# Kernel tuning notes

Measured on AMD Instinct MI355X. Metric: run time of the kernel, lower is better.

## Reference

```python
import jax, jax.numpy as jnp
import numpy as np

T = 131072  # timesteps
D = 256     # state_dim


def setup_inputs() -> dict:
    key = jax.random.key(0)
    kA, kB = jax.random.split(key)
    A = jax.random.normal(kA, (T, D), dtype=jnp.float32)
    Bu = jax.random.normal(kB, (T, D), dtype=jnp.float32)
    return {"A": A, "Bu": Bu}


def reference(A, Bu):
    # S5 associative scan combinator over (A, Bu) pairs along time axis 0:
    #   (A_i, Bu_i) * (A_j, Bu_j) = (A_j * A_i, A_j * Bu_i + Bu_j)
    def s5_operator(x, y):
        A_i, Bu_i = x
        A_j, Bu_j = y
        return (A_j * A_i, A_j * Bu_i + Bu_j)

    return jax.lax.associative_scan(s5_operator, (A, Bu), axis=0)
```

## Files before the change

### kernel.cpp

```cpp
#include <hip/hip_runtime.h>


#define T_TOTAL 131072
#define D_DIM   256
#define CHUNK   32
#define NCHUNK  (T_TOTAL / CHUNK)
#define NSUPER  64
#define SLEN    (NCHUNK / NSUPER)
#define NTHR    (D_DIM / 4)

typedef float vfloat4 __attribute__((ext_vector_type(4)));

__device__ __forceinline__ void combine(float4& ra, float4& rb,
                                        const float4 ga, const float4 gb) {
    rb.x = fmaf(ga.x, rb.x, gb.x);  ra.x = ga.x * ra.x;
    rb.y = fmaf(ga.y, rb.y, gb.y);  ra.y = ga.y * ra.y;
    rb.z = fmaf(ga.z, rb.z, gb.z);  ra.z = ga.z * ra.z;
    rb.w = fmaf(ga.w, rb.w, gb.w);  ra.w = ga.w * ra.w;
}

__device__ __forceinline__ void nt_store4(float* p, const float4 v) {
    vfloat4 t = {v.x, v.y, v.z, v.w};
    __builtin_nontemporal_store(t, (vfloat4*)p);
}

__global__ __launch_bounds__(NTHR) void s5_pass1(
    const float* __restrict__ A, const float* __restrict__ Bu,
    float* __restrict__ aggA, float* __restrict__ aggB)
{
    const int c  = blockIdx.x;
    const int ch = threadIdx.x * 4;
    const size_t base = (size_t)c * CHUNK * D_DIM + ch;

    float4 a = make_float4(1.f, 1.f, 1.f, 1.f);
    float4 b = make_float4(0.f, 0.f, 0.f, 0.f);

    #pragma unroll 8
    for (int t = 0; t < CHUNK; ++t) {
        const float4 at = *(const float4*)(A  + base + (size_t)t * D_DIM);
        const float4 bt = *(const float4*)(Bu + base + (size_t)t * D_DIM);
        combine(a, b, at, bt);
    }
    *(float4*)(aggA + (size_t)c * D_DIM + ch) = a;
    *(float4*)(aggB + (size_t)c * D_DIM + ch) = b;
}

__global__ __launch_bounds__(NTHR) void s5_pass2a(
    float* __restrict__ aggA, float* __restrict__ aggB,
    float* __restrict__ supA, float* __restrict__ supB)
{
    const int s  = blockIdx.x;
    const int ch = threadIdx.x * 4;

    float4 ra = make_float4(1.f, 1.f, 1.f, 1.f);
    float4 rb = make_float4(0.f, 0.f, 0.f, 0.f);

    for (int i = 0; i < SLEN; ++i) {
        const size_t o = (size_t)(s * SLEN + i) * D_DIM + ch;
        const float4 ga = *(const float4*)(aggA + o);
        const float4 gb = *(const float4*)(aggB + o);
        *(float4*)(aggA + o) = ra;
        *(float4*)(aggB + o) = rb;
        combine(ra, rb, ga, gb);
    }
    *(float4*)(supA + (size_t)s * D_DIM + ch) = ra;
    *(float4*)(supB + (size_t)s * D_DIM + ch) = rb;
}

__global__ __launch_bounds__(NTHR) void s5_pass2b(
    float* __restrict__ supA, float* __restrict__ supB)
{
    const int ch = threadIdx.x * 4;
    float4 ra = make_float4(1.f, 1.f, 1.f, 1.f);
    float4 rb = make_float4(0.f, 0.f, 0.f, 0.f);

    for (int s = 0; s < NSUPER; ++s) {
        const size_t o = (size_t)s * D_DIM + ch;
        const float4 ga = *(const float4*)(supA + o);
        const float4 gb = *(const float4*)(supB + o);
        *(float4*)(supA + o) = ra;
        *(float4*)(supB + o) = rb;
        combine(ra, rb, ga, gb);
    }
}

__global__ __launch_bounds__(NTHR) void s5_pass3(
    const float* __restrict__ A, const float* __restrict__ Bu,
    const float* __restrict__ relA, const float* __restrict__ relB,
    const float* __restrict__ supA, const float* __restrict__ supB,
    float* __restrict__ outA, float* __restrict__ outB)
{
    const int c  = blockIdx.x;
    const int ch = threadIdx.x * 4;
    const int s  = c / SLEN;

    const size_t co = (size_t)c * D_DIM + ch;
    const size_t so = (size_t)s * D_DIM + ch;

    const float4 rA = *(const float4*)(relA + co);
    const float4 rB = *(const float4*)(relB + co);
    const float4 sA = *(const float4*)(supA + so);
    const float4 sB = *(const float4*)(supB + so);

    float4 ra, rb;
    rb.x = fmaf(rA.x, sB.x, rB.x);  ra.x = rA.x * sA.x;
    rb.y = fmaf(rA.y, sB.y, rB.y);  ra.y = rA.y * sA.y;
    rb.z = fmaf(rA.z, sB.z, rB.z);  ra.z = rA.z * sA.z;
    rb.w = fmaf(rA.w, sB.w, rB.w);  ra.w = rA.w * sA.w;

    const size_t base = (size_t)c * CHUNK * D_DIM + ch;

    #pragma unroll 8
    for (int t = 0; t < CHUNK; ++t) {
        const size_t o = base + (size_t)t * D_DIM;
        const float4 at = *(const float4*)(A  + o);
        const float4 bt = *(const float4*)(Bu + o);
        combine(ra, rb, at, bt);
        nt_store4(outA + o, ra);
        nt_store4(outB + o, rb);
    }
}

extern "C" void kernel_launch(void* const* d_in, const int* in_sizes, int n_in,
                              void* d_out, int out_size, void* d_ws, size_t ws_size,
                              hipStream_t stream)
{
    const float* A  = (const float*)d_in[0];
    const float* Bu = (const float*)d_in[1];
    float* outA = (float*)d_out;
    float* outB = (float*)d_out + (size_t)T_TOTAL * D_DIM;

    float* aggA = (float*)d_ws;
    float* aggB = aggA + (size_t)NCHUNK * D_DIM;
    float* supA = aggB + (size_t)NCHUNK * D_DIM;
    float* supB = supA + (size_t)NSUPER * D_DIM;

    s5_pass1 <<<NCHUNK, NTHR, 0, stream>>>(A, Bu, aggA, aggB);
    s5_pass2a<<<NSUPER, NTHR, 0, stream>>>(aggA, aggB, supA, supB);
    s5_pass2b<<<1,      NTHR, 0, stream>>>(supA, supB);
    s5_pass3 <<<NCHUNK, NTHR, 0, stream>>>(A, Bu, aggA, aggB, supA, supB, outA, outB);
}
```

Measured before the change: 492.3 us.

## Replace three-pass scan with single-pass decoupled look-back scan

```diff
diff --git a/kernel.cpp b/kernel.cpp
--- a/kernel.cpp
+++ b/kernel.cpp
@@ -3,121 +3,172 @@
 
 #define T_TOTAL 131072
 #define D_DIM   256
-#define CHUNK   32
-#define NCHUNK  (T_TOTAL / CHUNK)
-#define NSUPER  64
-#define SLEN    (NCHUNK / NSUPER)
-#define NTHR    (D_DIM / 4)
+#define RPW     16
+#define WAVES   4
+#define RPB     (RPW * WAVES)
+#define NCHUNK  (T_TOTAL / RPB)
+#define NTHR    (WAVES * 64)
+
+#define F_NONE 0
+#define F_AGG  1
+#define F_PRE  2
 
 typedef float vfloat4 __attribute__((ext_vector_type(4)));
 
-__device__ __forceinline__ void combine(float4& ra, float4& rb,
-                                        const float4 ga, const float4 gb) {
-    rb.x = fmaf(ga.x, rb.x, gb.x);  ra.x = ga.x * ra.x;
-    rb.y = fmaf(ga.y, rb.y, gb.y);  ra.y = ga.y * ra.y;
-    rb.z = fmaf(ga.z, rb.z, gb.z);  ra.z = ga.z * ra.z;
-    rb.w = fmaf(ga.w, rb.w, gb.w);  ra.w = ga.w * ra.w;
+__device__ __forceinline__ float4 nt_load4(const float* p) {
+    vfloat4 t = __builtin_nontemporal_load((const vfloat4*)p);
+    return make_float4(t.x, t.y, t.z, t.w);
 }
-
 __device__ __forceinline__ void nt_store4(float* p, const float4 v) {
     vfloat4 t = {v.x, v.y, v.z, v.w};
     __builtin_nontemporal_store(t, (vfloat4*)p);
 }
 
-__global__ __launch_bounds__(NTHR) void s5_pass1(
-    const float* __restrict__ A, const float* __restrict__ Bu,
-    float* __restrict__ aggA, float* __restrict__ aggB)
-{
-    const int c  = blockIdx.x;
-    const int ch = threadIdx.x * 4;
-    const size_t base = (size_t)c * CHUNK * D_DIM + ch;
-
-    float4 a = make_float4(1.f, 1.f, 1.f, 1.f);
-    float4 b = make_float4(0.f, 0.f, 0.f, 0.f);
-
-    #pragma unroll 8
-    for (int t = 0; t < CHUNK; ++t) {
-        const float4 at = *(const float4*)(A  + base + (size_t)t * D_DIM);
-        const float4 bt = *(const float4*)(Bu + base + (size_t)t * D_DIM);
-        combine(a, b, at, bt);
-    }
-    *(float4*)(aggA + (size_t)c * D_DIM + ch) = a;
-    *(float4*)(aggB + (size_t)c * D_DIM + ch) = b;
+__device__ __forceinline__ void append(float4& ra, float4& rb,
+                                       const float4 ga, const float4 gb) {
+    rb.x = fmaf(ga.x, rb.x, gb.x);  ra.x *= ga.x;
+    rb.y = fmaf(ga.y, rb.y, gb.y);  ra.y *= ga.y;
+    rb.z = fmaf(ga.z, rb.z, gb.z);  ra.z *= ga.z;
+    rb.w = fmaf(ga.w, rb.w, gb.w);  ra.w *= ga.w;
+}
+__device__ __forceinline__ void prepend(float4& aa, float4& ab,
+                                        const float4 ga, const float4 gb) {
+    ab.x = fmaf(aa.x, gb.x, ab.x);  aa.x *= ga.x;
+    ab.y = fmaf(aa.y, gb.y, ab.y);  aa.y *= ga.y;
+    ab.z = fmaf(aa.z, gb.z, ab.z);  aa.z *= ga.z;
+    ab.w = fmaf(aa.w, gb.w, ab.w);  aa.w *= ga.w;
 }
 
-__global__ __launch_bounds__(NTHR) void s5_pass2a(
-    float* __restrict__ aggA, float* __restrict__ aggB,
-    float* __restrict__ supA, float* __restrict__ supB)
+__global__ __launch_bounds__(256) void s5_init(int* __restrict__ flags)
 {
-    const int s  = blockIdx.x;
-    const int ch = threadIdx.x * 4;
-
-    float4 ra = make_float4(1.f, 1.f, 1.f, 1.f);
-    float4 rb = make_float4(0.f, 0.f, 0.f, 0.f);
-
-    for (int i = 0; i < SLEN; ++i) {
-        const size_t o = (size_t)(s * SLEN + i) * D_DIM + ch;
-        const float4 ga = *(const float4*)(aggA + o);
-        const float4 gb = *(const float4*)(aggB + o);
-        *(float4*)(aggA + o) = ra;
-        *(float4*)(aggB + o) = rb;
-        combine(ra, rb, ga, gb);
-    }
-    *(float4*)(supA + (size_t)s * D_DIM + ch) = ra;
-    *(float4*)(supB + (size_t)s * D_DIM + ch) = rb;
+    const int i = blockIdx.x * 256 + threadIdx.x;
+    if (i <= NCHUNK) flags[i] = F_NONE;
 }
 
-__global__ __launch_bounds__(NTHR) void s5_pass2b(
-    float* __restrict__ supA, float* __restrict__ supB)
+__global__ __launch_bounds__(NTHR, 2) void s5_scan(
+    const float* __restrict__ A, const float* __restrict__ Bu,
+    float* __restrict__ outA, float* __restrict__ outB,
+    float* __restrict__ aggA, float* __restrict__ aggB,
+    float* __restrict__ preA, float* __restrict__ preB,
+    int* __restrict__ flags, int* __restrict__ ticket)
 {
-    const int ch = threadIdx.x * 4;
-    float4 ra = make_float4(1.f, 1.f, 1.f, 1.f);
-    float4 rb = make_float4(0.f, 0.f, 0.f, 0.f);
+    __shared__ float lsA[WAVES][D_DIM];
+    __shared__ float lsB[WAVES][D_DIM];
+    __shared__ float lpA[D_DIM];
+    __shared__ float lpB[D_DIM];
+    __shared__ int   s_chunk;
 
-    for (int s = 0; s < NSUPER; ++s) {
-        const size_t o = (size_t)s * D_DIM + ch;
-        const float4 ga = *(const float4*)(supA + o);
-        const float4 gb = *(const float4*)(supB + o);
-        *(float4*)(supA + o) = ra;
-        *(float4*)(supB + o) = rb;
-        combine(ra, rb, ga, gb);
+    const int tid  = threadIdx.x;
+    if (tid == 0) s_chunk = atomicAdd(ticket, 1);
+    __syncthreads();
+    const int chunk = s_chunk;
+    const int wave  = tid >> 6;
+    const int lane  = tid & 63;
+    const int ch    = lane * 4;
+
+    const size_t base = (size_t)(chunk * RPB + wave * RPW) * D_DIM + ch;
+
+    float4 la[RPW], lb[RPW];
+    #pragma unroll
+    for (int t = 0; t < RPW; ++t) {
+        la[t] = nt_load4(A  + base + (size_t)t * D_DIM);
+        lb[t] = nt_load4(Bu + base + (size_t)t * D_DIM);
     }
-}
 
-__global__ __launch_bounds__(NTHR) void s5_pass3(
-    const float* __restrict__ A, const float* __restrict__ Bu,
-    const float* __restrict__ relA, const float* __restrict__ relB,
-    const float* __restrict__ supA, const float* __restrict__ supB,
-    float* __restrict__ outA, float* __restrict__ outB)
-{
-    const int c  = blockIdx.x;
-    const int ch = threadIdx.x * 4;
-    const int s  = c / SLEN;
+    #pragma unroll
+    for (int t = 1; t < RPW; ++t) {
+        lb[t].x = fmaf(la[t].x, lb[t-1].x, lb[t].x);  la[t].x *= la[t-1].x;
+        lb[t].y = fmaf(la[t].y, lb[t-1].y, lb[t].y);  la[t].y *= la[t-1].y;
+        lb[t].z = fmaf(la[t].z, lb[t-1].z, lb[t].z);  la[t].z *= la[t-1].z;
+        lb[t].w = fmaf(la[t].w, lb[t-1].w, lb[t].w);  la[t].w *= la[t-1].w;
+    }
 
-    const size_t co = (size_t)c * D_DIM + ch;
-    const size_t so = (size_t)s * D_DIM + ch;
+    *(float4*)&lsA[wave][ch] = la[RPW - 1];
+    *(float4*)&lsB[wave][ch] = lb[RPW - 1];
+    __syncthreads();
 
-    const float4 rA = *(const float4*)(relA + co);
-    const float4 rB = *(const float4*)(relB + co);
-    const float4 sA = *(const float4*)(supA + so);
-    const float4 sB = *(const float4*)(supB + so);
+    float4 wpa = make_float4(1.f, 1.f, 1.f, 1.f);
+    float4 wpb = make_float4(0.f, 0.f, 0.f, 0.f);
+    #pragma unroll
+    for (int w = 0; w < WAVES - 1; ++w) {
+        if (wave > w)
+            append(wpa, wpb, *(const float4*)&lsA[w][ch],
+                             *(const float4*)&lsB[w][ch]);
+    }
 
-    float4 ra, rb;
-    rb.x = fmaf(rA.x, sB.x, rB.x);  ra.x = rA.x * sA.x;
-    rb.y = fmaf(rA.y, sB.y, rB.y);  ra.y = rA.y * sA.y;
-    rb.z = fmaf(rA.z, sB.z, rB.z);  ra.z = rA.z * sA.z;
-    rb.w = fmaf(rA.w, sB.w, rB.w);  ra.w = rA.w * sA.w;
+    if (wave == 3 && chunk > 0) {
+        float4 ba = wpa, bb = wpb;
+        append(ba, bb, la[RPW - 1], lb[RPW - 1]);
+        *(float4*)(aggA + (size_t)chunk * D_DIM + ch) = ba;
+        *(float4*)(aggB + (size_t)chunk * D_DIM + ch) = bb;
+        __threadfence();
+        if (lane == 0)
+            __hip_atomic_fetch_max(&flags[chunk], F_AGG,
+                                   __ATOMIC_RELEASE, __HIP_MEMORY_SCOPE_AGENT);
+    }
 
-    const size_t base = (size_t)c * CHUNK * D_DIM + ch;
+    if (wave == 0) {
+        float4 ba = make_float4(1.f, 1.f, 1.f, 1.f);
+        float4 bb = make_float4(0.f, 0.f, 0.f, 0.f);
+        #pragma unroll
+        for (int w = 0; w < WAVES; ++w)
+            append(ba, bb, *(const float4*)&lsA[w][ch],
+                           *(const float4*)&lsB[w][ch]);
 
-    #pragma unroll 8
-    for (int t = 0; t < CHUNK; ++t) {
-        const size_t o = base + (size_t)t * D_DIM;
-        const float4 at = *(const float4*)(A  + o);
-        const float4 bt = *(const float4*)(Bu + o);
-        combine(ra, rb, at, bt);
-        nt_store4(outA + o, ra);
-        nt_store4(outB + o, rb);
+        float4 Pa = make_float4(1.f, 1.f, 1.f, 1.f);
+        float4 Pb = make_float4(0.f, 0.f, 0.f, 0.f);
+        if (chunk > 0) {
+            int k = chunk - 1;
+            for (;;) {
+                int f;
+                for (;;) {
+                    f = __hip_atomic_load(&flags[k], __ATOMIC_ACQUIRE,
+                                          __HIP_MEMORY_SCOPE_AGENT);
+                    f = __builtin_amdgcn_readfirstlane(f);
+                    if (f != F_NONE) break;
+                    __builtin_amdgcn_s_sleep(1);
+                }
+                if (f == F_AGG) {
+                    const float4 ga = *(const float4*)(aggA + (size_t)k * D_DIM + ch);
+                    const float4 gb = *(const float4*)(aggB + (size_t)k * D_DIM + ch);
+                    prepend(Pa, Pb, ga, gb);
+                    --k;
+                } else {
+                    const float4 ga = *(const float4*)(preA + (size_t)k * D_DIM + ch);
+                    const float4 gb = *(const float4*)(preB + (size_t)k * D_DIM + ch);
+                    prepend(Pa, Pb, ga, gb);
+                    break;
+                }
+            }
+        }
+
+        float4 ia = Pa, ib = Pb;
+        append(ia, ib, ba, bb);
+        *(float4*)(preA + (size_t)chunk * D_DIM + ch) = ia;
+        *(float4*)(preB + (size_t)chunk * D_DIM + ch) = ib;
+        __threadfence();
+        if (lane == 0)
+            __hip_atomic_fetch_max(&flags[chunk], F_PRE,
+                                   __ATOMIC_RELEASE, __HIP_MEMORY_SCOPE_AGENT);
+
+        *(float4*)&lpA[ch] = Pa;
+        *(float4*)&lpB[ch] = Pb;
+    }
+    __syncthreads();
+
+    float4 fpA = *(const float4*)&lpA[ch];
+    float4 fpB = *(const float4*)&lpB[ch];
+    append(fpA, fpB, wpa, wpb);
+
+    #pragma unroll
+    for (int t = 0; t < RPW; ++t) {
+        float4 oa, ob;
+        oa.x = la[t].x * fpA.x;  ob.x = fmaf(la[t].x, fpB.x, lb[t].x);
+        oa.y = la[t].y * fpA.y;  ob.y = fmaf(la[t].y, fpB.y, lb[t].y);
+        oa.z = la[t].z * fpA.z;  ob.z = fmaf(la[t].z, fpB.z, lb[t].z);
+        oa.w = la[t].w * fpA.w;  ob.w = fmaf(la[t].w, fpB.w, lb[t].w);
+        nt_store4(outA + base + (size_t)t * D_DIM, oa);
+        nt_store4(outB + base + (size_t)t * D_DIM, ob);
     }
 }
 
@@ -128,15 +179,16 @@
     const float* A  = (const float*)d_in[0];
     const float* Bu = (const float*)d_in[1];
     float* outA = (float*)d_out;
-    float* outB = (float*)d_out + (size_t)T_TOTAL * D_DIM;
+    float* outB = outA + (size_t)T_TOTAL * D_DIM;
 
-    float* aggA = (float*)d_ws;
-    float* aggB = aggA + (size_t)NCHUNK * D_DIM;
-    float* supA = aggB + (size_t)NCHUNK * D_DIM;
-    float* supB = supA + (size_t)NSUPER * D_DIM;
+    float* aggA  = (float*)d_ws;
+    float* aggB  = aggA + (size_t)NCHUNK * D_DIM;
+    float* preA  = aggB + (size_t)NCHUNK * D_DIM;
+    float* preB  = preA + (size_t)NCHUNK * D_DIM;
+    int*   flags = (int*)(preB + (size_t)NCHUNK * D_DIM);
 
-    s5_pass1 <<<NCHUNK, NTHR, 0, stream>>>(A, Bu, aggA, aggB);
-    s5_pass2a<<<NSUPER, NTHR, 0, stream>>>(aggA, aggB, supA, supB);
-    s5_pass2b<<<1,      NTHR, 0, stream>>>(supA, supB);
-    s5_pass3 <<<NCHUNK, NTHR, 0, stream>>>(A, Bu, aggA, aggB, supA, supB, outA, outB);
+    s5_init<<<(NCHUNK + 1 + 255) / 256, 256, 0, stream>>>(flags);
+    s5_scan<<<NCHUNK, NTHR, 0, stream>>>(A, Bu, outA, outB,
+                                         aggA, aggB, preA, preB,
+                                         flags, flags + NCHUNK);
 }
```

Result: slower. 1.157 ms (+135.0%).
